# Optimization experiments

Measured on AMD Instinct MI355X. Metric: run time of the kernel, lower is better.

## Reference

```python
import jax, jax.numpy as jnp
import numpy as np

N_HEAD = 16


def setup_inputs() -> dict:
    key = jax.random.key(0)
    ks = jax.random.split(key, 6)
    B, T, C = 2, 2048, 1024
    hs = C // N_HEAD  # 64
    block_minus_1 = 2048  # block_size - 1
    x = jax.random.normal(ks[0], (B, T, C), dtype=jnp.float32)
    W1 = jax.random.normal(ks[1], (C, C), dtype=jnp.float32) * (1.0 / np.sqrt(C))
    b1 = jnp.zeros((C,), dtype=jnp.float32)
    # original init: uniform(-1e-3, 1e-3)
    w2 = jax.random.uniform(ks[2], (hs, block_minus_1), dtype=jnp.float32, minval=-1e-3, maxval=1e-3)
    b2 = jnp.zeros((block_minus_1,), dtype=jnp.float32)
    Wv = jax.random.normal(ks[3], (C, C), dtype=jnp.float32) * (1.0 / np.sqrt(C))
    bv = jnp.zeros((C,), dtype=jnp.float32)
    Wp = jax.random.normal(ks[4], (C, C), dtype=jnp.float32) * (1.0 / np.sqrt(C))
    bp = jnp.zeros((C,), dtype=jnp.float32)
    return {"x": x, "W1": W1, "b1": b1, "w2": w2, "b2": b2,
            "Wv": Wv, "bv": bv, "Wp": Wp, "bp": bp}


def reference(x, W1, b1, w2, b2, Wv, bv, Wp, bp):
    B, T, C = x.shape
    hs = C // N_HEAD
    r = jax.nn.relu(x @ W1.T + b1).reshape(B, T, N_HEAD, hs).transpose(0, 2, 1, 3)
    # synthesizer scores: (B, nh, T, T) = relu_out @ w2[:, :T] + b2[:T]
    att = jnp.einsum('bhtd,dj->bhtj', r, w2[:, :T]) + b2[:T]
    causal = jnp.tril(jnp.ones((T, T), dtype=bool))
    att = jnp.where(causal[None, None], att, jnp.float32(-1e10))
    att = jax.nn.softmax(att, axis=-1)  # attn_drop = 0 (eval)
    v = (x @ Wv.T + bv).reshape(B, T, N_HEAD, hs).transpose(0, 2, 1, 3)
    y = jnp.einsum('bhtj,bhjd->bhtd', att, v)
    y = y.transpose(0, 2, 1, 3).reshape(B, T, C)
    return y @ Wp.T + bp  # resid_drop = 0 (eval)
```

## Files before the change

### kernel.cpp

```cpp
#include <hip/hip_runtime.h>

typedef __bf16 bf16x8 __attribute__((ext_vector_type(8)));
typedef float f32x4 __attribute__((ext_vector_type(4)));

__device__ __forceinline__ unsigned short f2bf(float f) {
  union { float f; unsigned u; } v; v.f = f;
  unsigned u = v.u;
  return (unsigned short)((u + 0x7fffu + ((u >> 16) & 1u)) >> 16);
}
__device__ __forceinline__ unsigned short f2bf_fast(float f) {
  union { float f; unsigned u; } v; v.f = f;
  return (unsigned short)((v.u + 0x8000u) >> 16);
}
__device__ __forceinline__ void gload_lds16(const void* g, void* l) {
  __builtin_amdgcn_global_load_lds(
      (const __attribute__((address_space(1))) unsigned int*)g,
      (__attribute__((address_space(3))) unsigned int*)l, 16, 0, 0);
}
__device__ __forceinline__ void cvt4(const float* __restrict__ s,
                                     unsigned short* __restrict__ d, int u) {
  f32x4 v = ((const f32x4*)s)[u];
  union { unsigned short s[4]; unsigned long long u; } o;
  o.s[0] = f2bf(v[0]); o.s[1] = f2bf(v[1]); o.s[2] = f2bf(v[2]); o.s[3] = f2bf(v[3]);
  ((unsigned long long*)d)[u] = o.u;
}


__global__ void prep(const float* __restrict__ x, const float* __restrict__ W1,
                     const float* __restrict__ Wv, const float* __restrict__ Wp,
                     const float* __restrict__ w2, const float* __restrict__ b2,
                     unsigned short* __restrict__ xb, unsigned short* __restrict__ W1b,
                     unsigned short* __restrict__ Wvb, unsigned short* __restrict__ Wpb,
                     unsigned short* __restrict__ w2t, unsigned short* __restrict__ ebj) {
  int u = blockIdx.x * 256 + threadIdx.x;
  if (u < 1048576) { cvt4(x, xb, u); return; }
  u -= 1048576;
  if (u < 262144) { cvt4(W1, W1b, u); return; }
  u -= 262144;
  if (u < 262144) { cvt4(Wv, Wvb, u); return; }
  u -= 262144;
  if (u < 262144) { cvt4(Wp, Wpb, u); return; }
  u -= 262144;
  if (u < 32768) {
    int j = u >> 4, d4 = (u & 15) * 4;
    union { unsigned short s[4]; unsigned long long x; } o;
#pragma unroll
    for (int i = 0; i < 4; ++i) o.s[i] = f2bf(w2[(d4 + i) * 2048 + j]);
    ((unsigned long long*)w2t)[u] = o.x;
    return;
  }
  u -= 32768;
  union { unsigned short s[4]; unsigned long long x; } o;
#pragma unroll
  for (int i = 0; i < 4; ++i) o.s[i] = f2bf(__expf(b2[u * 4 + i]));
  ((unsigned long long*)ebj)[u] = o.x;
}

__global__ __launch_bounds__(256) void gemm_rv(
    const unsigned short* __restrict__ xb, const unsigned short* __restrict__ W1b,
    const unsigned short* __restrict__ Wvb, const float* __restrict__ b1,
    const float* __restrict__ bv, const float* __restrict__ b2,
    unsigned short* __restrict__ rb, unsigned short* __restrict__ vtb) {
  __shared__ unsigned short Xs[64 * 64];
  __shared__ unsigned short W1s[64 * 64];
  __shared__ unsigned short Wvs[64 * 64];
  const int tm = blockIdx.x * 64, n0 = blockIdx.y * 64;
  const int tid = threadIdx.x;
  const int wv = tid >> 6, ln = tid & 63;
  const int quad = ln >> 4, lq = ln & 15;
  const int rowL = ln >> 3;
  const int kc = (((ln & 7) ^ rowL) & 7) * 8;
  const int sx = lq & 7;
  const int ko0 = (quad ^ sx) * 8, ko1 = ((4 + quad) ^ sx) * 8;

  f32x4 accR[4], accV[4];
  const f32x4 zf = {0.f, 0.f, 0.f, 0.f};
#pragma unroll
  for (int j = 0; j < 4; ++j) { accR[j] = zf; accV[j] = zf; }

  for (int k0 = 0; k0 < 1024; k0 += 64) {
    __syncthreads();
#pragma unroll
    for (int l = 0; l < 2; ++l) {
      int row = l * 32 + wv * 8 + rowL;
      gload_lds16(xb + (tm + row) * 1024 + k0 + kc, &Xs[l * 2048 + wv * 512]);
      gload_lds16(W1b + (n0 + row) * 1024 + k0 + kc, &W1s[l * 2048 + wv * 512]);
      gload_lds16(Wvb + (n0 + row) * 1024 + k0 + kc, &Wvs[l * 2048 + wv * 512]);
    }
    __syncthreads();
#pragma unroll
    for (int kk = 0; kk < 2; ++kk) {
      const int ko = kk ? ko1 : ko0;
      bf16x8 xa  = *(const bf16x8*)&Xs[(wv * 16 + lq) * 64 + ko];
      bf16x8 wva = *(const bf16x8*)&Wvs[(wv * 16 + lq) * 64 + ko];
#pragma unroll
      for (int ni = 0; ni < 4; ++ni) {
        bf16x8 w1f = *(const bf16x8*)&W1s[(ni * 16 + lq) * 64 + ko];
        accR[ni] = __builtin_amdgcn_mfma_f32_16x16x32_bf16(xa, w1f, accR[ni], 0, 0, 0);
      }
#pragma unroll
      for (int nj = 0; nj < 4; ++nj) {
        bf16x8 xbf = *(const bf16x8*)&Xs[(nj * 16 + lq) * 64 + ko];
        accV[nj] = __builtin_amdgcn_mfma_f32_16x16x32_bf16(wva, xbf, accV[nj], 0, 0, 0);
      }
    }
  }
#pragma unroll
  for (int ni = 0; ni < 4; ++ni) {
    int col = n0 + ni * 16 + lq;
    float bc = b1[col];
#pragma unroll
    for (int rg = 0; rg < 4; ++rg) {
      int row = tm + wv * 16 + quad * 4 + rg;
      float v = accR[ni][rg] + bc;
      rb[row * 1024 + col] = f2bf(v > 0.f ? v : 0.f);
    }
  }
  float bvv[4];
#pragma unroll
  for (int rg = 0; rg < 4; ++rg) bvv[rg] = bv[n0 + wv * 16 + quad * 4 + rg];
#pragma unroll
  for (int nj = 0; nj < 4; ++nj) {
    int tok = tm + nj * 16 + lq;
    float eb = __expf(b2[tok & 2047]);
#pragma unroll
    for (int rg = 0; rg < 4; ++rg) {
      int ch = n0 + wv * 16 + quad * 4 + rg;
      vtb[ch * 4096 + tok] = f2bf((accV[nj][rg] + bvv[rg]) * eb);
    }
  }
}

__global__ __launch_bounds__(256) void gemm_p(
    const unsigned short* __restrict__ A, const unsigned short* __restrict__ Bt,
    const float* __restrict__ bias, float* __restrict__ C) {
  __shared__ unsigned short As[64 * 128];
  __shared__ unsigned short Bs[64 * 128];
  const int tid = threadIdx.x;
  const int wv = tid >> 6, ln = tid & 63;
  const int quad = ln >> 4, lq = ln & 15;
  const int tileM = blockIdx.y * 64, tileN = blockIdx.x * 64;
  const int srow = ln >> 4, pos = ln & 15;

  f32x4 acc[4];
  const f32x4 zf = {0.f, 0.f, 0.f, 0.f};
#pragma unroll
  for (int j = 0; j < 4; ++j) acc[j] = zf;

  int kof[4];
#pragma unroll
  for (int kk = 0; kk < 4; ++kk) {
    int c = kk * 4 + quad;
    kof[kk] = (((c & 8) | ((c & 7) ^ (lq & 7)))) * 8;
  }

  for (int k0 = 0; k0 < 1024; k0 += 128) {
    __syncthreads();
#pragma unroll
    for (int l = 0; l < 4; ++l) {
      int row = l * 16 + wv * 4 + srow;
      int cs = (pos & 8) | ((pos & 7) ^ (row & 7));
      gload_lds16(A + (tileM + row) * 1024 + k0 + cs * 8, &As[(l * 16 + wv * 4) * 128]);
      gload_lds16(Bt + (tileN + row) * 1024 + k0 + cs * 8, &Bs[(l * 16 + wv * 4) * 128]);
    }
    __syncthreads();
#pragma unroll
    for (int kk = 0; kk < 4; ++kk) {
      const int ko = kof[kk];
      bf16x8 af = *(const bf16x8*)&As[(wv * 16 + lq) * 128 + ko];
#pragma unroll
      for (int ni = 0; ni < 4; ++ni) {
        bf16x8 bfr = *(const bf16x8*)&Bs[(ni * 16 + lq) * 128 + ko];
        acc[ni] = __builtin_amdgcn_mfma_f32_16x16x32_bf16(af, bfr, acc[ni], 0, 0, 0);
      }
    }
  }
#pragma unroll
  for (int ni = 0; ni < 4; ++ni) {
    int col = tileN + ni * 16 + lq;
#pragma unroll
    for (int rg = 0; rg < 4; ++rg) {
      int row = tileM + wv * 16 + quad * 4 + rg;
      C[row * 1024 + col] = acc[ni][rg] + bias[col];
    }
  }
}

__global__ __launch_bounds__(256, 2) void attn(
    const unsigned short* __restrict__ r, const unsigned short* __restrict__ w2t,
    const unsigned short* __restrict__ vt, const unsigned short* __restrict__ ebj,
    unsigned short* __restrict__ y) {
  __shared__ unsigned short W2s[2][64 * 64];
  __shared__ unsigned short Vs[2][64 * 64];
  __shared__ unsigned short Ps[4][16 * 64];

  const int tid = threadIdx.x;
  const int wv = tid >> 6, ln = tid & 63;
  const int quad = ln >> 4, lq = ln & 15;
  const int bh = blockIdx.x, b = bh >> 4, h = bh & 15;
  const int q = blockIdx.y;
  const int p = (q < 8) ? q : 23 - q;
  const int ta = p, tb = 31 - p;
  const int t0a = ta * 64, t0b = tb * 64;
  const int rowL = ln >> 3;
  const int kc = (((ln & 7) ^ rowL) & 7) * 8;
  const int sx = lq & 7;
  const int ko0 = (quad ^ sx) * 8, ko1 = ((4 + quad) ^ sx) * 8;

  bf16x8 ra[2][2];
  {
    const unsigned short* base = r + (b * 2048 + wv * 16 + lq) * 1024 + h * 64 + quad * 8;
    ra[0][0] = *(const bf16x8*)(base + t0a * 1024);
    ra[0][1] = *(const bf16x8*)(base + t0a * 1024 + 32);
    ra[1][0] = *(const bf16x8*)(base + t0b * 1024);
    ra[1][1] = *(const bf16x8*)(base + t0b * 1024 + 32);
  }

  f32x4 accY[2][4];
  f32x4 accL[2];
  const f32x4 zf = {0.f, 0.f, 0.f, 0.f};
#pragma unroll
  for (int s = 0; s < 2; ++s) {
    accL[s] = zf;
#pragma unroll
    for (int nd = 0; nd < 4; ++nd) accY[s][nd] = zf;
  }

  auto stage = [&](int jt, int bi) {
    int j0 = jt * 64;
#pragma unroll
    for (int l = 0; l < 2; ++l) {
      int row = l * 32 + wv * 8 + rowL;
      gload_lds16(w2t + (j0 + row) * 64 + kc, &W2s[bi][l * 2048 + wv * 512]);
      gload_lds16(vt + (h * 64 + row) * 4096 + b * 2048 + j0 + kc,
                  &Vs[bi][l * 2048 + wv * 512]);
    }
  };

#define TILE(S, T0, TT)                                                         \
    {                                                                           \
      f32x4 sv[4] = {zf, zf, zf, zf};                                           \
      _Pragma("unroll") for (int ni = 0; ni < 4; ++ni) {                        \
        sv[ni] = __builtin_amdgcn_mfma_f32_16x16x32_bf16(ra[S][0], w2f0[ni], sv[ni], 0, 0, 0); \
        sv[ni] = __builtin_amdgcn_mfma_f32_16x16x32_bf16(ra[S][1], w2f1[ni], sv[ni], 0, 0, 0); \
      }                                                                         \
      const bool diag = (jt == (TT));                                           \
      _Pragma("unroll") for (int ni = 0; ni < 4; ++ni) {                        \
        int j = j0 + ni * 16 + lq;                                              \
        _Pragma("unroll") for (int rg = 0; rg < 4; ++rg) {                      \
          float pe = __expf(sv[ni][rg]);                                        \
          if (diag) {                                                           \
            int t = (T0) + wv * 16 + quad * 4 + rg;                             \
            pe = (j <= t) ? pe : 0.f;                                           \
          }                                                                     \
          Ps[wv][(quad * 4 + rg) * 64 +                                         \
                 (((ni * 2 + (lq >> 3)) ^ ((quad * 4 + rg) & 7)) * 8) + (lq & 7)] = f2bf_fast(pe); \
        }                                                                       \
      }                                                                         \
      _Pragma("unroll") for (int kk = 0; kk < 2; ++kk) {                        \
        const int ko = kk ? ko1 : ko0;                                          \
        bf16x8 pa = *(const bf16x8*)&Ps[wv][lq * 64 + ko];                      \
        _Pragma("unroll") for (int nd = 0; nd < 4; ++nd) {                      \
          bf16x8 bb = *(const bf16x8*)&Vs[cb][(nd * 16 + lq) * 64 + ko];        \
          accY[S][nd] = __builtin_amdgcn_mfma_f32_16x16x32_bf16(pa, bb, accY[S][nd], 0, 0, 0); \
        }                                                                       \
        accL[S] = __builtin_amdgcn_mfma_f32_16x16x32_bf16(pa, kk ? eb1 : eb0, accL[S], 0, 0, 0); \
      }                                                                         \
    }

#define WRITEOUT(S, T0)                                                         \
    {                                                                           \
      float inv[4];                                                             \
      _Pragma("unroll") for (int rg = 0; rg < 4; ++rg)                          \
        inv[rg] = __builtin_amdgcn_rcpf(accL[S][rg]);                           \
      _Pragma("unroll") for (int nd = 0; nd < 4; ++nd)                          \
        _Pragma("unroll") for (int rg = 0; rg < 4; ++rg) {                      \
          int t = (T0) + wv * 16 + quad * 4 + rg;                               \
          y[(b * 2048 + t) * 1024 + h * 64 + nd * 16 + lq] =                    \
              f2bf(accY[S][nd][rg] * inv[rg]);                                  \
        }                                                                       \
    }

  stage(0, 0);
  for (int jt = 0; jt <= tb; ++jt) {
    const int cb = jt & 1;
    __syncthreads();
    if (jt < tb) stage(jt + 1, cb ^ 1);
    const int j0 = jt * 64;

    bf16x8 eb0 = *(const bf16x8*)&ebj[j0 + quad * 8];
    bf16x8 eb1 = *(const bf16x8*)&ebj[j0 + 32 + quad * 8];
    bf16x8 w2f0[4], w2f1[4];
#pragma unroll
    for (int ni = 0; ni < 4; ++ni) {
      w2f0[ni] = *(const bf16x8*)&W2s[cb][(ni * 16 + lq) * 64 + ko0];
      w2f1[ni] = *(const bf16x8*)&W2s[cb][(ni * 16 + lq) * 64 + ko1];
    }

    if (jt <= ta) TILE(0, t0a, ta);
    TILE(1, t0b, tb);
    if (jt == ta) WRITEOUT(0, t0a);
  }
  WRITEOUT(1, t0b);
#undef TILE
#undef WRITEOUT
}

extern "C" void kernel_launch(void* const* d_in, const int* in_sizes, int n_in,
                              void* d_out, int out_size, void* d_ws, size_t ws_size,
                              hipStream_t stream) {
  const float* x  = (const float*)d_in[0];
  const float* W1 = (const float*)d_in[1];
  const float* b1 = (const float*)d_in[2];
  const float* w2 = (const float*)d_in[3];
  const float* b2 = (const float*)d_in[4];
  const float* Wv = (const float*)d_in[5];
  const float* bv = (const float*)d_in[6];
  const float* Wp = (const float*)d_in[7];
  const float* bp = (const float*)d_in[8];

  unsigned short* ws  = (unsigned short*)d_ws;
  unsigned short* xb   = ws;
  unsigned short* W1b  = ws + 4194304;
  unsigned short* Wvb  = ws + 5242880;
  unsigned short* Wpb  = ws + 6291456;
  unsigned short* w2t  = ws + 7340032;
  unsigned short* rb   = ws + 7471104;
  unsigned short* vt   = ws + 11665408;
  unsigned short* yb   = ws + 15859712;
  unsigned short* ebjb = ws + 20054016;

  prep<<<7298, 256, 0, stream>>>(x, W1, Wv, Wp, w2, b2, xb, W1b, Wvb, Wpb, w2t, ebjb);
  gemm_rv<<<dim3(64, 16), 256, 0, stream>>>(xb, W1b, Wvb, b1, bv, b2, rb, vt);
  attn<<<dim3(32, 16), 256, 0, stream>>>(rb, w2t, vt, ebjb, yb);
  gemm_p<<<dim3(16, 64), 256, 0, stream>>>(yb, Wpb, bp, (float*)d_out);
}
```

Measured before the change: 170.3 us.

## Enlarge rv GEMM token tile, store relu output transposed, interleave attention tiles

The fused R/V projection GEMM now covers 128 tokens per block and shares each X fragment between the W1 and Wv MFMAs. It writes the relu output channel-major (transposed), matching the V layout, and the grid is halved. The attention kernel gathers its r fragments element by element from the transposed layout and interleaves the two query tiles' score, exp and PV stages using separate P buffers, which should expose more MFMA parallelism. The risks are strided scalar gathers for r, higher register pressure from 16 accumulators per thread in the GEMM, and fewer blocks in flight.

```diff
diff --git a/kernel.cpp b/kernel.cpp
--- a/kernel.cpp
+++ b/kernel.cpp
@@ -60,11 +60,11 @@
     const unsigned short* __restrict__ xb, const unsigned short* __restrict__ W1b,
     const unsigned short* __restrict__ Wvb, const float* __restrict__ b1,
     const float* __restrict__ bv, const float* __restrict__ b2,
-    unsigned short* __restrict__ rb, unsigned short* __restrict__ vtb) {
-  __shared__ unsigned short Xs[64 * 64];
+    unsigned short* __restrict__ rT, unsigned short* __restrict__ vtb) {
+  __shared__ unsigned short Xs[128 * 64];
   __shared__ unsigned short W1s[64 * 64];
   __shared__ unsigned short Wvs[64 * 64];
-  const int tm = blockIdx.x * 64, n0 = blockIdx.y * 64;
+  const int tm = blockIdx.x * 128, n0 = blockIdx.y * 64;
   const int tid = threadIdx.x;
   const int wv = tid >> 6, ln = tid & 63;
   const int quad = ln >> 4, lq = ln & 15;
@@ -73,17 +73,21 @@
   const int sx = lq & 7;
   const int ko0 = (quad ^ sx) * 8, ko1 = ((4 + quad) ^ sx) * 8;
 
-  f32x4 accR[4], accV[4];
+  f32x4 accR[8], accV[8];
   const f32x4 zf = {0.f, 0.f, 0.f, 0.f};
 #pragma unroll
-  for (int j = 0; j < 4; ++j) { accR[j] = zf; accV[j] = zf; }
+  for (int j = 0; j < 8; ++j) { accR[j] = zf; accV[j] = zf; }
 
   for (int k0 = 0; k0 < 1024; k0 += 64) {
     __syncthreads();
+#pragma unroll
+    for (int l = 0; l < 4; ++l) {
+      int row = l * 32 + wv * 8 + rowL;
+      gload_lds16(xb + (tm + row) * 1024 + k0 + kc, &Xs[l * 2048 + wv * 512]);
+    }
 #pragma unroll
     for (int l = 0; l < 2; ++l) {
       int row = l * 32 + wv * 8 + rowL;
-      gload_lds16(xb + (tm + row) * 1024 + k0 + kc, &Xs[l * 2048 + wv * 512]);
       gload_lds16(W1b + (n0 + row) * 1024 + k0 + kc, &W1s[l * 2048 + wv * 512]);
       gload_lds16(Wvb + (n0 + row) * 1024 + k0 + kc, &Wvs[l * 2048 + wv * 512]);
     }
@@ -91,41 +95,31 @@
 #pragma unroll
     for (int kk = 0; kk < 2; ++kk) {
       const int ko = kk ? ko1 : ko0;
-      bf16x8 xa  = *(const bf16x8*)&Xs[(wv * 16 + lq) * 64 + ko];
+      bf16x8 w1a = *(const bf16x8*)&W1s[(wv * 16 + lq) * 64 + ko];
       bf16x8 wva = *(const bf16x8*)&Wvs[(wv * 16 + lq) * 64 + ko];
 #pragma unroll
-      for (int ni = 0; ni < 4; ++ni) {
-        bf16x8 w1f = *(const bf16x8*)&W1s[(ni * 16 + lq) * 64 + ko];
-        accR[ni] = __builtin_amdgcn_mfma_f32_16x16x32_bf16(xa, w1f, accR[ni], 0, 0, 0);
-      }
-#pragma unroll
-      for (int nj = 0; nj < 4; ++nj) {
-        bf16x8 xbf = *(const bf16x8*)&Xs[(nj * 16 + lq) * 64 + ko];
-        accV[nj] = __builtin_amdgcn_mfma_f32_16x16x32_bf16(wva, xbf, accV[nj], 0, 0, 0);
-      }
-    }
-  }
-#pragma unroll
-  for (int ni = 0; ni < 4; ++ni) {
-    int col = n0 + ni * 16 + lq;
-    float bc = b1[col];
-#pragma unroll
-    for (int rg = 0; rg < 4; ++rg) {
-      int row = tm + wv * 16 + quad * 4 + rg;
-      float v = accR[ni][rg] + bc;
-      rb[row * 1024 + col] = f2bf(v > 0.f ? v : 0.f);
-    }
-  }
-  float bvv[4];
-#pragma unroll
-  for (int rg = 0; rg < 4; ++rg) bvv[rg] = bv[n0 + wv * 16 + quad * 4 + rg];
-#pragma unroll
-  for (int nj = 0; nj < 4; ++nj) {
+      for (int nj = 0; nj < 8; ++nj) {
+        bf16x8 xf = *(const bf16x8*)&Xs[(nj * 16 + lq) * 64 + ko];
+        accR[nj] = __builtin_amdgcn_mfma_f32_16x16x32_bf16(w1a, xf, accR[nj], 0, 0, 0);
+        accV[nj] = __builtin_amdgcn_mfma_f32_16x16x32_bf16(wva, xf, accV[nj], 0, 0, 0);
+      }
+    }
+  }
+  float b1v[4], bvv[4];
+#pragma unroll
+  for (int rg = 0; rg < 4; ++rg) {
+    b1v[rg] = b1[n0 + wv * 16 + quad * 4 + rg];
+    bvv[rg] = bv[n0 + wv * 16 + quad * 4 + rg];
+  }
+#pragma unroll
+  for (int nj = 0; nj < 8; ++nj) {
     int tok = tm + nj * 16 + lq;
     float eb = __expf(b2[tok & 2047]);
 #pragma unroll
     for (int rg = 0; rg < 4; ++rg) {
       int ch = n0 + wv * 16 + quad * 4 + rg;
+      float rv = accR[nj][rg] + b1v[rg];
+      rT[ch * 4096 + tok] = f2bf(rv > 0.f ? rv : 0.f);
       vtb[ch * 4096 + tok] = f2bf((accV[nj][rg] + bvv[rg]) * eb);
     }
   }
@@ -187,12 +181,12 @@
 }
 
 __global__ __launch_bounds__(256, 2) void attn(
-    const unsigned short* __restrict__ r, const unsigned short* __restrict__ w2t,
+    const unsigned short* __restrict__ rT, const unsigned short* __restrict__ w2t,
     const unsigned short* __restrict__ vt, const unsigned short* __restrict__ ebj,
     unsigned short* __restrict__ y) {
   __shared__ unsigned short W2s[2][64 * 64];
   __shared__ unsigned short Vs[2][64 * 64];
-  __shared__ unsigned short Ps[4][16 * 64];
+  __shared__ unsigned short Ps[4][2][16 * 64];
 
   const int tid = threadIdx.x;
   const int wv = tid >> 6, ln = tid & 63;
@@ -209,11 +203,16 @@
 
   bf16x8 ra[2][2];
   {
-    const unsigned short* base = r + (b * 2048 + wv * 16 + lq) * 1024 + h * 64 + quad * 8;
-    ra[0][0] = *(const bf16x8*)(base + t0a * 1024);
-    ra[0][1] = *(const bf16x8*)(base + t0a * 1024 + 32);
-    ra[1][0] = *(const bf16x8*)(base + t0b * 1024);
-    ra[1][1] = *(const bf16x8*)(base + t0b * 1024 + 32);
+    const unsigned short* base = rT + (h * 64 + quad * 8) * 4096 + b * 2048 + wv * 16 + lq;
+#pragma unroll
+    for (int s = 0; s < 2; ++s) {
+      int t0s = s ? t0b : t0a;
+#pragma unroll
+      for (int i = 0; i < 8; ++i) {
+        ra[s][0][i] = *(const __bf16*)&base[i * 4096 + t0s];
+        ra[s][1][i] = *(const __bf16*)&base[(32 + i) * 4096 + t0s];
+      }
+    }
   }
 
   f32x4 accY[2][4];
@@ -236,37 +235,6 @@
                   &Vs[bi][l * 2048 + wv * 512]);
     }
   };
-
-#define TILE(S, T0, TT)                                                         \
-    {                                                                           \
-      f32x4 sv[4] = {zf, zf, zf, zf};                                           \
-      _Pragma("unroll") for (int ni = 0; ni < 4; ++ni) {                        \
-        sv[ni] = __builtin_amdgcn_mfma_f32_16x16x32_bf16(ra[S][0], w2f0[ni], sv[ni], 0, 0, 0); \
-        sv[ni] = __builtin_amdgcn_mfma_f32_16x16x32_bf16(ra[S][1], w2f1[ni], sv[ni], 0, 0, 0); \
-      }                                                                         \
-      const bool diag = (jt == (TT));                                           \
-      _Pragma("unroll") for (int ni = 0; ni < 4; ++ni) {                        \
-        int j = j0 + ni * 16 + lq;                                              \
-        _Pragma("unroll") for (int rg = 0; rg < 4; ++rg) {                      \
-          float pe = __expf(sv[ni][rg]);                                        \
-          if (diag) {                                                           \
-            int t = (T0) + wv * 16 + quad * 4 + rg;                             \
-            pe = (j <= t) ? pe : 0.f;                                           \
-          }                                                                     \
-          Ps[wv][(quad * 4 + rg) * 64 +                                         \
-                 (((ni * 2 + (lq >> 3)) ^ ((quad * 4 + rg) & 7)) * 8) + (lq & 7)] = f2bf_fast(pe); \
-        }                                                                       \
-      }                                                                         \
-      _Pragma("unroll") for (int kk = 0; kk < 2; ++kk) {                        \
-        const int ko = kk ? ko1 : ko0;                                          \
-        bf16x8 pa = *(const bf16x8*)&Ps[wv][lq * 64 + ko];                      \
-        _Pragma("unroll") for (int nd = 0; nd < 4; ++nd) {                      \
-          bf16x8 bb = *(const bf16x8*)&Vs[cb][(nd * 16 + lq) * 64 + ko];        \
-          accY[S][nd] = __builtin_amdgcn_mfma_f32_16x16x32_bf16(pa, bb, accY[S][nd], 0, 0, 0); \
-        }                                                                       \
-        accL[S] = __builtin_amdgcn_mfma_f32_16x16x32_bf16(pa, kk ? eb1 : eb0, accL[S], 0, 0, 0); \
-      }                                                                         \
-    }
 
 #define WRITEOUT(S, T0)                                                         \
     {                                                                           \
@@ -287,6 +255,7 @@
     __syncthreads();
     if (jt < tb) stage(jt + 1, cb ^ 1);
     const int j0 = jt * 64;
+    const bool act0 = (jt <= ta);
 
     bf16x8 eb0 = *(const bf16x8*)&ebj[j0 + quad * 8];
     bf16x8 eb1 = *(const bf16x8*)&ebj[j0 + 32 + quad * 8];
@@ -297,12 +266,78 @@
       w2f1[ni] = *(const bf16x8*)&W2s[cb][(ni * 16 + lq) * 64 + ko1];
     }
 
-    if (jt <= ta) TILE(0, t0a, ta);
-    TILE(1, t0b, tb);
+    f32x4 sv0[4] = {zf, zf, zf, zf};
+    f32x4 sv1[4] = {zf, zf, zf, zf};
+    if (act0) {
+#pragma unroll
+      for (int ni = 0; ni < 4; ++ni) {
+        sv0[ni] = __builtin_amdgcn_mfma_f32_16x16x32_bf16(ra[0][0], w2f0[ni], sv0[ni], 0, 0, 0);
+        sv0[ni] = __builtin_amdgcn_mfma_f32_16x16x32_bf16(ra[0][1], w2f1[ni], sv0[ni], 0, 0, 0);
+      }
+    }
+#pragma unroll
+    for (int ni = 0; ni < 4; ++ni) {
+      sv1[ni] = __builtin_amdgcn_mfma_f32_16x16x32_bf16(ra[1][0], w2f0[ni], sv1[ni], 0, 0, 0);
+      sv1[ni] = __builtin_amdgcn_mfma_f32_16x16x32_bf16(ra[1][1], w2f1[ni], sv1[ni], 0, 0, 0);
+    }
+
+    if (act0) {
+      const bool diag0 = (jt == ta);
+#pragma unroll
+      for (int ni = 0; ni < 4; ++ni) {
+        int j = j0 + ni * 16 + lq;
+#pragma unroll
+        for (int rg = 0; rg < 4; ++rg) {
+          float pe = __expf(sv0[ni][rg]);
+          if (diag0) {
+            int t = t0a + wv * 16 + quad * 4 + rg;
+            pe = (j <= t) ? pe : 0.f;
+          }
+          Ps[wv][0][(quad * 4 + rg) * 64 +
+                    (((ni * 2 + (lq >> 3)) ^ ((quad * 4 + rg) & 7)) * 8) + (lq & 7)] = f2bf_fast(pe);
+        }
+      }
+    }
+    {
+      const bool diag1 = (jt == tb);
+#pragma unroll
+      for (int ni = 0; ni < 4; ++ni) {
+        int j = j0 + ni * 16 + lq;
+#pragma unroll
+        for (int rg = 0; rg < 4; ++rg) {
+          float pe = __expf(sv1[ni][rg]);
+          if (diag1) {
+            int t = t0b + wv * 16 + quad * 4 + rg;
+            pe = (j <= t) ? pe : 0.f;
+          }
+          Ps[wv][1][(quad * 4 + rg) * 64 +
+                    (((ni * 2 + (lq >> 3)) ^ ((quad * 4 + rg) & 7)) * 8) + (lq & 7)] = f2bf_fast(pe);
+        }
+      }
+    }
+
+#pragma unroll
+    for (int kk = 0; kk < 2; ++kk) {
+      const int ko = kk ? ko1 : ko0;
+      bf16x8 pa1 = *(const bf16x8*)&Ps[wv][1][lq * 64 + ko];
+      bf16x8 pa0;
+      if (act0) pa0 = *(const bf16x8*)&Ps[wv][0][lq * 64 + ko];
+#pragma unroll
+      for (int nd = 0; nd < 4; ++nd) {
+        bf16x8 bb = *(const bf16x8*)&Vs[cb][(nd * 16 + lq) * 64 + ko];
+        accY[1][nd] = __builtin_amdgcn_mfma_f32_16x16x32_bf16(pa1, bb, accY[1][nd], 0, 0, 0);
+        if (act0)
+          accY[0][nd] = __builtin_amdgcn_mfma_f32_16x16x32_bf16(pa0, bb, accY[0][nd], 0, 0, 0);
+      }
+      bf16x8 ebk = kk ? eb1 : eb0;
+      accL[1] = __builtin_amdgcn_mfma_f32_16x16x32_bf16(pa1, ebk, accL[1], 0, 0, 0);
+      if (act0)
+        accL[0] = __builtin_amdgcn_mfma_f32_16x16x32_bf16(pa0, ebk, accL[0], 0, 0, 0);
+    }
+
     if (jt == ta) WRITEOUT(0, t0a);
   }
   WRITEOUT(1, t0b);
-#undef TILE
 #undef WRITEOUT
 }
 
@@ -325,13 +360,13 @@
   unsigned short* Wvb  = ws + 5242880;
   unsigned short* Wpb  = ws + 6291456;
   unsigned short* w2t  = ws + 7340032;
-  unsigned short* rb   = ws + 7471104;
+  unsigned short* rT   = ws + 7471104;
   unsigned short* vt   = ws + 11665408;
   unsigned short* yb   = ws + 15859712;
   unsigned short* ebjb = ws + 20054016;
 
   prep<<<7298, 256, 0, stream>>>(x, W1, Wv, Wp, w2, b2, xb, W1b, Wvb, Wpb, w2t, ebjb);
-  gemm_rv<<<dim3(64, 16), 256, 0, stream>>>(xb, W1b, Wvb, b1, bv, b2, rb, vt);
-  attn<<<dim3(32, 16), 256, 0, stream>>>(rb, w2t, vt, ebjb, yb);
+  gemm_rv<<<dim3(32, 16), 256, 0, stream>>>(xb, W1b, Wvb, b1, bv, b2, rT, vt);
+  attn<<<dim3(32, 16), 256, 0, stream>>>(rT, w2t, vt, ebjb, yb);
   gemm_p<<<dim3(16, 64), 256, 0, stream>>>(yb, Wpb, bp, (float*)d_out);
 }
```

Result: slower. 181.7 us (+6.7%).
